# Performance work log

Measured on AMD Instinct MI355X. Metric: run time of the kernel, lower is better.

The kernel has to match this reference:

```python
import jax, jax.numpy as jnp
import numpy as np

NUM_LAYERS = 4
CODEBOOK_SIZE = 2048
DIM = 256
N = 32768
BETA = 0.25
EPS = 1e-12  # F.normalize eps


def setup_inputs() -> dict:
    key = jax.random.key(0)
    kx, kc = jax.random.split(key)
    x = jax.random.normal(kx, (N, DIM), dtype=jnp.float32)
    # nn.Embedding default init: N(0, 1)
    codebooks = jax.random.normal(kc, (NUM_LAYERS, CODEBOOK_SIZE, DIM), dtype=jnp.float32)
    return {"x": x, "codebooks": codebooks}


def reference(x, codebooks):
    sg = jax.lax.stop_gradient
    residual = x
    all_indices = []
    decoded = jnp.zeros_like(x)
    total_loss = jnp.zeros((), dtype=x.dtype)
    n_elem = x.size
    for layer in range(NUM_LAYERS):
        cb = codebooks[layer]                      # [K, D] (raw, used for gather)
        norm = jnp.linalg.norm(cb, axis=-1, keepdims=True)
        cbn = cb / jnp.maximum(norm, EPS)          # L2-normalized, used for distances
        # squared L2 distances; argmin is invariant to the sqrt in torch.cdist
        d2 = (
            jnp.sum(residual * residual, axis=-1, keepdims=True)
            - 2.0 * residual @ cbn.T
            + jnp.sum(cbn * cbn, axis=-1)
        )                                          # [N, K]
        idx = jnp.argmin(d2, axis=-1)              # [N]
        all_indices.append(idx)
        q = cb[idx]                                # [N, D] gather from RAW codebook
        codebook_loss = jnp.sum((residual - sg(q)) ** 2) / n_elem
        commitment_loss = jnp.sum((sg(residual) - q) ** 2) / n_elem
        total_loss = total_loss + codebook_loss + BETA * commitment_loss
        decoded = decoded + q
        # residual = residual - (residual + sg(q - residual)) == sg(residual - q)
        residual = sg(residual - q)
    stru_ids = jnp.stack(all_indices, axis=1)      # [N, L]
    return stru_ids, decoded, total_loss
```

## Files before the change

### kernel.cpp

```cpp
#include <hip/hip_runtime.h>
#include <math.h>

#define L_NUM 4
#define K_CB  2048
#define D_DIM 256
#define N_ROWS 32768
#define CAP 56
#define WACC  0.12f
#define WACC2 0.125f

typedef _Float16 half8 __attribute__((ext_vector_type(8)));
typedef _Float16 half4v __attribute__((ext_vector_type(4)));
typedef float f32x16 __attribute__((ext_vector_type(16)));

__device__ __forceinline__ void gl_lds16(const void* g, void* l) {
  __builtin_amdgcn_global_load_lds(
      (const __attribute__((address_space(1))) void*)g,
      (__attribute__((address_space(3))) void*)l, 16, 0, 0);
}
__device__ __forceinline__ unsigned fenc(float f) {
  unsigned u = __float_as_uint(f);
  return (u & 0x80000000u) ? ~u : (u | 0x80000000u);
}
__device__ __forceinline__ float fdec(unsigned k) {
  unsigned u = (k & 0x80000000u) ? (k ^ 0x80000000u) : ~k;
  return __uint_as_float(u);
}

__global__ __launch_bounds__(64)
void prep_all_kernel(const float* __restrict__ cb,
                     float* __restrict__ cbn,
                     _Float16* __restrict__ cb16) {
  const int b = blockIdx.x;
  const int k = b & 2047, l = b >> 11;
  const int lane = threadIdx.x;
  float4 v = reinterpret_cast<const float4*>(cb + (size_t)b * D_DIM)[lane];
  float s = v.x*v.x + v.y*v.y + v.z*v.z + v.w*v.w;
  #pragma unroll
  for (int m = 1; m < 64; m <<= 1) s += __shfl_xor(s, m, 64);
  const float den = fmaxf(sqrtf(s), 1e-12f);
  v.x /= den; v.y /= den; v.z /= den; v.w /= den;
  reinterpret_cast<float4*>(cbn + (size_t)b * D_DIM)[lane] = v;
  half4v h;
  h[0] = (_Float16)v.x; h[1] = (_Float16)v.y; h[2] = (_Float16)v.z; h[3] = (_Float16)v.w;
  const int tile = k >> 9, col = k & 511;
  const int kchunk = lane >> 3;
  const int sslot  = (lane >> 1) & 3;
  const int rem    = (lane & 1) * 4;
  const size_t off = (size_t)l * (K_CB * D_DIM)
                   + (size_t)(tile * 8 + kchunk) * 16384
                   + (size_t)sslot * 4096 + (size_t)col * 8 + rem;
  *(half4v*)(cb16 + off) = h;
}

__global__ __launch_bounds__(512, 2)
void rq_fused_kernel(const float* __restrict__ x,
                     const float* __restrict__ cb,
                     const float* __restrict__ cbn,
                     const _Float16* __restrict__ cb16,
                     float* __restrict__ out_ids,
                     float* __restrict__ out_dec,
                     double* __restrict__ dloss) {
  extern __shared__ char sm[];
  _Float16* A16   = (_Float16*)sm;
  _Float16* Bs    = (_Float16*)(sm + 65536);
  unsigned* cp    = (unsigned*)(sm + 131072);
  int*      cn    = (int*)(sm + 131072 + 128*CAP*4);
  unsigned* gmax  = (unsigned*)((char*)cn + 512);
  unsigned* bestp = (unsigned*)((char*)gmax + 512);

  const int t = threadIdx.x;
  const int wid = t >> 6, ln = t & 63;
  const int l31 = ln & 31, hl = ln >> 5;
  const int rowg = wid >> 2, colg = wid & 3;
  const int urow = t >> 2, qo = (t & 3) * 64;
  const int row0 = blockIdx.x * 128;
  const int mrow0 = rowg * 64 + l31, mrow1 = mrow0 + 32;

  float r[64];
  {
    const float4* xg = (const float4*)(x + (size_t)(row0 + urow) * D_DIM + qo);
    #pragma unroll
    for (int i = 0; i < 16; ++i) {
      const float4 a = xg[i];
      r[i*4+0]=a.x; r[i*4+1]=a.y; r[i*4+2]=a.z; r[i*4+3]=a.w;
    }
  }
  #pragma unroll
  for (int j = 0; j < 8; ++j) {
    half8 h;
    #pragma unroll
    for (int e = 0; e < 8; ++e) h[e] = (_Float16)r[j*8+e];
    const int slot = (t & 3) * 8 + j;
    *(half8*)(A16 + slot*1024 + urow*8) = h;
  }
  if (t < 128) { cn[t] = 0; gmax[t] = 0u; bestp[t] = 0u; }
  int id0 = 0, id1 = 0, id2 = 0, id3 = 0;
  double lloss = 0.0;

  #pragma unroll 1
  for (int l = 0; l < L_NUM; ++l) {
    const char* Bimg = (const char*)cb16 + (size_t)l * (K_CB * D_DIM * 2);
    {
      char* dst = (char*)Bs;
      #pragma unroll
      for (int i = 0; i < 4; ++i)
        gl_lds16(Bimg + t*16 + i*8192, dst + t*16 + i*8192);
    }
    __syncthreads();

    f32x16 acc[4][2];

    #pragma unroll 1
    for (int g = 0; g < 32; ++g) {
      if ((g & 7) == 0) {
        #pragma unroll
        for (int bi = 0; bi < 4; ++bi)
          #pragma unroll
          for (int ai = 0; ai < 2; ++ai)
            #pragma unroll
            for (int e = 0; e < 16; ++e) acc[bi][ai][e] = 0.f;
      }
      if (g < 31) {
        char* dst = (char*)Bs + ((g + 1) & 1) * 32768;
        const char* src = Bimg + (size_t)(g + 1) * 32768;
        #pragma unroll
        for (int i = 0; i < 4; ++i)
          gl_lds16(src + t*16 + i*8192, dst + t*16 + i*8192);
      }
      const _Float16* Bb = Bs + (g & 1) * 16384;
      const int cK = g & 7;
      #pragma unroll
      for (int ks2 = 0; ks2 < 2; ++ks2) {
        const int sa = cK*4 + ks2*2 + hl;
        const int sb = ks2*2 + hl;
        half8 af[2], bf[4];
        af[0] = *(const half8*)(A16 + sa*1024 + mrow0*8);
        af[1] = *(const half8*)(A16 + sa*1024 + mrow1*8);
        #pragma unroll
        for (int bi = 0; bi < 4; ++bi) {
          const int col = colg*128 + bi*32 + l31;
          bf[bi] = *(const half8*)(Bb + sb*4096 + col*8);
        }
        #pragma unroll
        for (int bi = 0; bi < 4; ++bi) {
          acc[bi][0] = __builtin_amdgcn_mfma_f32_32x32x16_f16(bf[bi], af[0], acc[bi][0], 0, 0, 0);
          acc[bi][1] = __builtin_amdgcn_mfma_f32_32x32x16_f16(bf[bi], af[1], acc[bi][1], 0, 0, 0);
        }
      }
      if ((g & 7) == 7) {
        const int ct = g >> 3;
        #pragma unroll
        for (int ai = 0; ai < 2; ++ai) {
          const int mrow = ai ? mrow1 : mrow0;
          float m = -INFINITY;
          #pragma unroll
          for (int bi = 0; bi < 4; ++bi)
            #pragma unroll
            for (int rg = 0; rg < 16; ++rg) m = fmaxf(m, acc[bi][ai][rg]);
          atomicMax(&gmax[mrow], fenc(m));
          const float thr = fdec(gmax[mrow]) - WACC;
          #pragma unroll
          for (int bi = 0; bi < 4; ++bi)
            #pragma unroll
            for (int rg = 0; rg < 16; ++rg) {
              const float v = acc[bi][ai][rg];
              if (v >= thr) {
                const unsigned q = (unsigned)((v + 64.f) * 16384.f);
                const unsigned cidx = (unsigned)(ct*512 + colg*128 + bi*32
                                                 + 4*hl + (rg & 3) + 8*(rg >> 2));
                const unsigned pk = (q << 11) | cidx;
                atomicMax(&bestp[mrow], pk);
                const int slot = atomicAdd(&cn[mrow], 1);
                if (slot < CAP) cp[mrow*CAP + slot] = pk;
              }
            }
        }
      }
      __syncthreads();
    }

    {
      const float thr2 = fdec(gmax[urow]) - WACC2;
      const int m = min(cn[urow], CAP);
      double bsc = (double)INFINITY; int bidx = 0x7fffffff;
      #pragma unroll 1
      for (int j = 0; j <= m; ++j) {
        const unsigned p = (j < m) ? cp[urow*CAP + j] : bestp[urow];
        const float v = (float)(p >> 11) * (1.f/16384.f) - 64.f;
        if (j < m && v < thr2) continue;
        const int cidx = (int)(p & 2047u);
        const float4* cpn = (const float4*)(cbn + ((size_t)l*K_CB + cidx)*D_DIM + qo);
        double s = 0.0, n2 = 0.0;
        #pragma unroll
        for (int i = 0; i < 16; ++i) {
          const float4 a = cpn[i];
          s  = fma((double)r[i*4+0], (double)a.x, s);
          s  = fma((double)r[i*4+1], (double)a.y, s);
          s  = fma((double)r[i*4+2], (double)a.z, s);
          s  = fma((double)r[i*4+3], (double)a.w, s);
          n2 = fma((double)a.x, (double)a.x, n2);
          n2 = fma((double)a.y, (double)a.y, n2);
          n2 = fma((double)a.z, (double)a.z, n2);
          n2 = fma((double)a.w, (double)a.w, n2);
        }
        s  += __shfl_xor(s, 1, 64);  s  += __shfl_xor(s, 2, 64);
        n2 += __shfl_xor(n2, 1, 64); n2 += __shfl_xor(n2, 2, 64);
        const double sc = -2.0 * s + n2;
        if (sc < bsc || (sc == bsc && cidx < bidx)) { bsc = sc; bidx = cidx; }
      }
      bidx &= 2047;
      if (l == 0) id0 = bidx; else if (l == 1) id1 = bidx;
      else if (l == 2) id2 = bidx; else id3 = bidx;
      if ((t & 3) == 0) out_ids[(size_t)(row0 + urow)*L_NUM + l] = (float)bidx;

      const float4* qg = (const float4*)(cb + ((size_t)l*K_CB + bidx)*D_DIM + qo);
      #pragma unroll
      for (int i = 0; i < 16; ++i) {
        const float4 q = qg[i];
        r[i*4+0] -= q.x; r[i*4+1] -= q.y; r[i*4+2] -= q.z; r[i*4+3] -= q.w;
        lloss += (double)r[i*4+0]*r[i*4+0] + (double)r[i*4+1]*r[i*4+1]
               + (double)r[i*4+2]*r[i*4+2] + (double)r[i*4+3]*r[i*4+3];
      }
      if (l < 3) {
        #pragma unroll
        for (int j = 0; j < 8; ++j) {
          half8 h;
          #pragma unroll
          for (int e = 0; e < 8; ++e) h[e] = (_Float16)r[j*8+e];
          const int slot = (t & 3) * 8 + j;
          *(half8*)(A16 + slot*1024 + urow*8) = h;
        }
      }
    }
    __syncthreads();
    if (l < 3 && t < 128) { cn[t] = 0; gmax[t] = 0u; bestp[t] = 0u; }
  }

  {
    float dec[64];
    #pragma unroll
    for (int l2 = 0; l2 < L_NUM; ++l2) {
      const int idl = (l2 == 0) ? id0 : (l2 == 1) ? id1 : (l2 == 2) ? id2 : id3;
      const float4* qg = (const float4*)(cb + ((size_t)l2*K_CB + idl)*D_DIM + qo);
      #pragma unroll
      for (int i = 0; i < 16; ++i) {
        const float4 q = qg[i];
        if (l2 == 0) { dec[i*4+0]=q.x; dec[i*4+1]=q.y; dec[i*4+2]=q.z; dec[i*4+3]=q.w; }
        else { dec[i*4+0]+=q.x; dec[i*4+1]+=q.y; dec[i*4+2]+=q.z; dec[i*4+3]+=q.w; }
      }
    }
    float4* dg = (float4*)(out_dec + (size_t)(row0 + urow)*D_DIM + qo);
    #pragma unroll
    for (int i = 0; i < 16; ++i)
      dg[i] = make_float4(dec[i*4+0], dec[i*4+1], dec[i*4+2], dec[i*4+3]);
  }

  double* lw = (double*)cp;
  #pragma unroll
  for (int m = 1; m < 64; m <<= 1) lloss += __shfl_xor(lloss, m, 64);
  if (ln == 0) lw[wid] = lloss;
  __syncthreads();
  if (t == 0) {
    double s2 = 0.0;
    #pragma unroll
    for (int j = 0; j < 8; ++j) s2 += lw[j];
    atomicAdd(dloss, s2);
  }
}

__global__ void rq_fin_kernel(const double* __restrict__ dls, float* __restrict__ out_loss) {
  out_loss[0] = (float)(dls[0] * 1.25 / 8388608.0);
}

extern "C" void kernel_launch(void* const* d_in, const int* in_sizes, int n_in,
                              void* d_out, int out_size, void* d_ws, size_t ws_size,
                              hipStream_t stream) {
  const float* x  = (const float*)d_in[0];
  const float* cb = (const float*)d_in[1];
  float* out      = (float*)d_out;
  float* out_ids  = out;
  float* out_dec  = out + (size_t)N_ROWS * L_NUM;
  float* out_loss = out_dec + (size_t)N_ROWS * D_DIM;

  char* w = (char*)d_ws;
  double* dls = (double*)w;                   w += 256;
  float* cbn = (float*)w;                     w += (size_t)L_NUM*K_CB*D_DIM*4;
  _Float16* cb16 = (_Float16*)w;              w += (size_t)L_NUM*K_CB*D_DIM*2;

  hipMemsetAsync(dls, 0, sizeof(double), stream);
  prep_all_kernel<<<L_NUM*K_CB, 64, 0, stream>>>(cb, cbn, cb16);

  const size_t smem = 65536 + 65536 + 128*CAP*4 + 512 + 512 + 512;
  hipFuncSetAttribute(reinterpret_cast<const void*>(rq_fused_kernel),
                      hipFuncAttributeMaxDynamicSharedMemorySize, (int)smem);
  rq_fused_kernel<<<N_ROWS/128, 512, smem, stream>>>(x, cb, cbn, cb16,
                                                     out_ids, out_dec, dls);
  rq_fin_kernel<<<1, 1, 0, stream>>>(dls, out_loss);
}
```

Before: 345.1 us.

## Halve block tile to 64 rows with 256 threads and 256-column B chunks

Reduces each block from 128 rows and 512 threads to 64 rows and 256 threads, with each wave computing a 32x128 tile (4 MFMA accumulators instead of 8). The codebook fp16 layout is reorganized into 256-column chunks of 16 KB, so the double-buffered B stage is halved and the loop runs 64 steps. Shared memory per block roughly halves and register pressure drops, which should allow more blocks per CU and better latency hiding. The cost is that every block still streams the full codebook per layer, so total L2/global traffic for B doubles and B reuse across rows halves, with more barriers per layer.

```diff
diff --git a/kernel.cpp b/kernel.cpp
--- a/kernel.cpp
+++ b/kernel.cpp
@@ -5,6 +5,7 @@
 #define K_CB  2048
 #define D_DIM 256
 #define N_ROWS 32768
+#define ROWS_B 64
 #define CAP 56
 #define WACC  0.12f
 #define WACC2 0.125f
@@ -43,17 +44,17 @@
   reinterpret_cast<float4*>(cbn + (size_t)b * D_DIM)[lane] = v;
   half4v h;
   h[0] = (_Float16)v.x; h[1] = (_Float16)v.y; h[2] = (_Float16)v.z; h[3] = (_Float16)v.w;
-  const int tile = k >> 9, col = k & 511;
-  const int kchunk = lane >> 3;
-  const int sslot  = (lane >> 1) & 3;
-  const int rem    = (lane & 1) * 4;
+  const int ct = k >> 8, col = k & 255;
+  const int kc    = lane >> 3;
+  const int sslot = (lane >> 1) & 3;
+  const int rem   = (lane & 1) * 4;
   const size_t off = (size_t)l * (K_CB * D_DIM)
-                   + (size_t)(tile * 8 + kchunk) * 16384
-                   + (size_t)sslot * 4096 + (size_t)col * 8 + rem;
+                   + (size_t)(ct * 8 + kc) * 8192
+                   + (size_t)sslot * 2048 + (size_t)col * 8 + rem;
   *(half4v*)(cb16 + off) = h;
 }
 
-__global__ __launch_bounds__(512, 2)
+__global__ __launch_bounds__(256, 2)
 void rq_fused_kernel(const float* __restrict__ x,
                      const float* __restrict__ cb,
                      const float* __restrict__ cbn,
@@ -63,19 +64,19 @@
                      double* __restrict__ dloss) {
   extern __shared__ char sm[];
   _Float16* A16   = (_Float16*)sm;
-  _Float16* Bs    = (_Float16*)(sm + 65536);
-  unsigned* cp    = (unsigned*)(sm + 131072);
-  int*      cn    = (int*)(sm + 131072 + 128*CAP*4);
-  unsigned* gmax  = (unsigned*)((char*)cn + 512);
-  unsigned* bestp = (unsigned*)((char*)gmax + 512);
+  _Float16* Bs    = (_Float16*)(sm + 32768);
+  unsigned* cp    = (unsigned*)(sm + 65536);
+  int*      cn    = (int*)(sm + 65536 + 64*CAP*4);
+  unsigned* gmax  = (unsigned*)((char*)cn + 256);
+  unsigned* bestp = (unsigned*)((char*)gmax + 256);
 
   const int t = threadIdx.x;
   const int wid = t >> 6, ln = t & 63;
   const int l31 = ln & 31, hl = ln >> 5;
-  const int rowg = wid >> 2, colg = wid & 3;
+  const int rowg = wid >> 1, colg = wid & 1;
   const int urow = t >> 2, qo = (t & 3) * 64;
-  const int row0 = blockIdx.x * 128;
-  const int mrow0 = rowg * 64 + l31, mrow1 = mrow0 + 32;
+  const int row0 = blockIdx.x * ROWS_B;
+  const int mrow = rowg * 32 + l31;
 
   float r[64];
   {
@@ -92,9 +93,9 @@
     #pragma unroll
     for (int e = 0; e < 8; ++e) h[e] = (_Float16)r[j*8+e];
     const int slot = (t & 3) * 8 + j;
-    *(half8*)(A16 + slot*1024 + urow*8) = h;
-  }
-  if (t < 128) { cn[t] = 0; gmax[t] = 0u; bestp[t] = 0u; }
+    *(half8*)(A16 + slot*512 + urow*8) = h;
+  }
+  if (t < 64) { cn[t] = 0; gmax[t] = 0u; bestp[t] = 0u; }
   int id0 = 0, id1 = 0, id2 = 0, id3 = 0;
   double lloss = 0.0;
 
@@ -105,77 +106,71 @@
       char* dst = (char*)Bs;
       #pragma unroll
       for (int i = 0; i < 4; ++i)
-        gl_lds16(Bimg + t*16 + i*8192, dst + t*16 + i*8192);
+        gl_lds16(Bimg + t*16 + i*4096, dst + t*16 + i*4096);
     }
     __syncthreads();
 
-    f32x16 acc[4][2];
+    f32x16 acc[4];
 
     #pragma unroll 1
-    for (int g = 0; g < 32; ++g) {
+    for (int g = 0; g < 64; ++g) {
       if ((g & 7) == 0) {
         #pragma unroll
         for (int bi = 0; bi < 4; ++bi)
           #pragma unroll
-          for (int ai = 0; ai < 2; ++ai)
-            #pragma unroll
-            for (int e = 0; e < 16; ++e) acc[bi][ai][e] = 0.f;
-      }
-      if (g < 31) {
-        char* dst = (char*)Bs + ((g + 1) & 1) * 32768;
-        const char* src = Bimg + (size_t)(g + 1) * 32768;
+          for (int e = 0; e < 16; ++e) acc[bi][e] = 0.f;
+      }
+      if (g < 63) {
+        char* dst = (char*)Bs + ((g + 1) & 1) * 16384;
+        const char* src = Bimg + (size_t)(g + 1) * 16384;
         #pragma unroll
         for (int i = 0; i < 4; ++i)
-          gl_lds16(src + t*16 + i*8192, dst + t*16 + i*8192);
-      }
-      const _Float16* Bb = Bs + (g & 1) * 16384;
-      const int cK = g & 7;
+          gl_lds16(src + t*16 + i*4096, dst + t*16 + i*4096);
+      }
+      const _Float16* Bb = Bs + (g & 1) * 8192;
+      const int kc = g & 7;
       #pragma unroll
       for (int ks2 = 0; ks2 < 2; ++ks2) {
-        const int sa = cK*4 + ks2*2 + hl;
         const int sb = ks2*2 + hl;
-        half8 af[2], bf[4];
-        af[0] = *(const half8*)(A16 + sa*1024 + mrow0*8);
-        af[1] = *(const half8*)(A16 + sa*1024 + mrow1*8);
-        #pragma unroll
-        for (int bi = 0; bi < 4; ++bi) {
-          const int col = colg*128 + bi*32 + l31;
-          bf[bi] = *(const half8*)(Bb + sb*4096 + col*8);
-        }
-        #pragma unroll
-        for (int bi = 0; bi < 4; ++bi) {
-          acc[bi][0] = __builtin_amdgcn_mfma_f32_32x32x16_f16(bf[bi], af[0], acc[bi][0], 0, 0, 0);
-          acc[bi][1] = __builtin_amdgcn_mfma_f32_32x32x16_f16(bf[bi], af[1], acc[bi][1], 0, 0, 0);
-        }
+        const int sa = kc*4 + sb;
+        const half8 af = *(const half8*)(A16 + sa*512 + mrow*8);
+        half8 bf[4];
+        #pragma unroll
+        for (int bi = 0; bi < 4; ++bi)
+          bf[bi] = *(const half8*)(Bb + sb*2048 + (colg*128 + bi*32 + l31)*8);
+        #pragma unroll
+        for (int bi = 0; bi < 4; ++bi)
+          acc[bi] = __builtin_amdgcn_mfma_f32_32x32x16_f16(bf[bi], af, acc[bi], 0, 0, 0);
       }
       if ((g & 7) == 7) {
         const int ct = g >> 3;
-        #pragma unroll
-        for (int ai = 0; ai < 2; ++ai) {
-          const int mrow = ai ? mrow1 : mrow0;
-          float m = -INFINITY;
+        float m4[4];
+        #pragma unroll
+        for (int bi = 0; bi < 4; ++bi) {
+          float m0 = fmaxf(fmaxf(acc[bi][0], acc[bi][1]), fmaxf(acc[bi][2], acc[bi][3]));
+          float m1 = fmaxf(fmaxf(acc[bi][4], acc[bi][5]), fmaxf(acc[bi][6], acc[bi][7]));
+          float m2 = fmaxf(fmaxf(acc[bi][8], acc[bi][9]), fmaxf(acc[bi][10], acc[bi][11]));
+          float m3 = fmaxf(fmaxf(acc[bi][12], acc[bi][13]), fmaxf(acc[bi][14], acc[bi][15]));
+          m4[bi] = fmaxf(fmaxf(m0, m1), fmaxf(m2, m3));
+        }
+        const float m = fmaxf(fmaxf(m4[0], m4[1]), fmaxf(m4[2], m4[3]));
+        atomicMax(&gmax[mrow], fenc(m));
+        const float thr = fdec(gmax[mrow]) - WACC;
+        #pragma unroll
+        for (int bi = 0; bi < 4; ++bi)
           #pragma unroll
-          for (int bi = 0; bi < 4; ++bi)
-            #pragma unroll
-            for (int rg = 0; rg < 16; ++rg) m = fmaxf(m, acc[bi][ai][rg]);
-          atomicMax(&gmax[mrow], fenc(m));
-          const float thr = fdec(gmax[mrow]) - WACC;
-          #pragma unroll
-          for (int bi = 0; bi < 4; ++bi)
-            #pragma unroll
-            for (int rg = 0; rg < 16; ++rg) {
-              const float v = acc[bi][ai][rg];
-              if (v >= thr) {
-                const unsigned q = (unsigned)((v + 64.f) * 16384.f);
-                const unsigned cidx = (unsigned)(ct*512 + colg*128 + bi*32
-                                                 + 4*hl + (rg & 3) + 8*(rg >> 2));
-                const unsigned pk = (q << 11) | cidx;
-                atomicMax(&bestp[mrow], pk);
-                const int slot = atomicAdd(&cn[mrow], 1);
-                if (slot < CAP) cp[mrow*CAP + slot] = pk;
-              }
+          for (int rg = 0; rg < 16; ++rg) {
+            const float v = acc[bi][rg];
+            if (v >= thr) {
+              const unsigned q = (unsigned)((v + 64.f) * 16384.f);
+              const unsigned cidx = (unsigned)(ct*256 + colg*128 + bi*32
+                                               + 4*hl + (rg & 3) + 8*(rg >> 2));
+              const unsigned pk = (q << 11) | cidx;
+              atomicMax(&bestp[mrow], pk);
+              const int slot = atomicAdd(&cn[mrow], 1);
+              if (slot < CAP) cp[mrow*CAP + slot] = pk;
             }
-        }
+          }
       }
       __syncthreads();
     }
@@ -229,12 +224,12 @@
           #pragma unroll
           for (int e = 0; e < 8; ++e) h[e] = (_Float16)r[j*8+e];
           const int slot = (t & 3) * 8 + j;
-          *(half8*)(A16 + slot*1024 + urow*8) = h;
+          *(half8*)(A16 + slot*512 + urow*8) = h;
         }
       }
     }
     __syncthreads();
-    if (l < 3 && t < 128) { cn[t] = 0; gmax[t] = 0u; bestp[t] = 0u; }
+    if (l < 3 && t < 64) { cn[t] = 0; gmax[t] = 0u; bestp[t] = 0u; }
   }
 
   {
@@ -261,12 +256,7 @@
   for (int m = 1; m < 64; m <<= 1) lloss += __shfl_xor(lloss, m, 64);
   if (ln == 0) lw[wid] = lloss;
   __syncthreads();
-  if (t == 0) {
-    double s2 = 0.0;
-    #pragma unroll
-    for (int j = 0; j < 8; ++j) s2 += lw[j];
-    atomicAdd(dloss, s2);
-  }
+  if (t == 0) atomicAdd(dloss, lw[0] + lw[1] + lw[2] + lw[3]);
 }
 
 __global__ void rq_fin_kernel(const double* __restrict__ dls, float* __restrict__ out_loss) {
@@ -291,10 +281,10 @@
   hipMemsetAsync(dls, 0, sizeof(double), stream);
   prep_all_kernel<<<L_NUM*K_CB, 64, 0, stream>>>(cb, cbn, cb16);
 
-  const size_t smem = 65536 + 65536 + 128*CAP*4 + 512 + 512 + 512;
+  const size_t smem = 32768 + 32768 + 64*CAP*4 + 256 + 256 + 256;
   hipFuncSetAttribute(reinterpret_cast<const void*>(rq_fused_kernel),
                       hipFuncAttributeMaxDynamicSharedMemorySize, (int)smem);
-  rq_fused_kernel<<<N_ROWS/128, 512, smem, stream>>>(x, cb, cbn, cb16,
-                                                     out_ids, out_dec, dls);
+  rq_fused_kernel<<<N_ROWS/ROWS_B, 256, smem, stream>>>(x, cb, cbn, cb16,
+                                                        out_ids, out_dec, dls);
   rq_fin_kernel<<<1, 1, 0, stream>>>(dls, out_loss);
 }
```

Measured after the change: 352.8 us. 2.2% more time.

## Drop persistent residual registers, recompute residual, use split barriers with vmcnt waits

Applied to the files above, without the earlier changes.

Stops keeping the 64-float residual in registers across the whole GEMM loop and instead reloads x and subtracts the previously chosen raw codebook rows before the refinement step, cutting register pressure during the MFMA loop. The per-tile __syncthreads is replaced with raw s_barrier pairs and explicit s_waitcnt vmcnt so the next tile's global-to-LDS prefetch stays in flight. Candidate capacity is lowered from 56 to 40 to shrink LDS. The cost is extra global reads of x and codebook rows per layer, plus a higher chance that the candidate list overflows.

```diff
diff --git a/kernel.cpp b/kernel.cpp
--- a/kernel.cpp
+++ b/kernel.cpp
@@ -5,7 +5,8 @@
 #define K_CB  2048
 #define D_DIM 256
 #define N_ROWS 32768
-#define CAP 56
+#define ROWS_B 128
+#define CAP 40
 #define WACC  0.12f
 #define WACC2 0.125f
 
@@ -43,14 +44,38 @@
   reinterpret_cast<float4*>(cbn + (size_t)b * D_DIM)[lane] = v;
   half4v h;
   h[0] = (_Float16)v.x; h[1] = (_Float16)v.y; h[2] = (_Float16)v.z; h[3] = (_Float16)v.w;
-  const int tile = k >> 9, col = k & 511;
-  const int kchunk = lane >> 3;
-  const int sslot  = (lane >> 1) & 3;
-  const int rem    = (lane & 1) * 4;
+  const int ct = k >> 9, col = k & 511;
+  const int kc    = lane >> 3;
+  const int sslot = (lane >> 1) & 3;
+  const int rem   = (lane & 1) * 4;
   const size_t off = (size_t)l * (K_CB * D_DIM)
-                   + (size_t)(tile * 8 + kchunk) * 16384
+                   + (size_t)(ct * 8 + kc) * 16384
                    + (size_t)sslot * 4096 + (size_t)col * 8 + rem;
   *(half4v*)(cb16 + off) = h;
+}
+
+#define COLL(ACC, BI, MROW, THR, CT) \
+  _Pragma("unroll") \
+  for (int rg = 0; rg < 16; ++rg) { \
+    const float v_ = (ACC)[rg]; \
+    if (v_ >= (THR)) { \
+      const unsigned q_ = (unsigned)((v_ + 64.f) * 16384.f); \
+      const unsigned ci_ = (unsigned)((CT)*512 + colg*128 + (BI)*32 \
+                                      + 4*hl + (rg & 3) + 8*(rg >> 2)); \
+      const unsigned pk_ = (q_ << 11) | ci_; \
+      atomicMax(&bestp[(MROW)], pk_); \
+      const int slot_ = atomicAdd(&cn[(MROW)], 1); \
+      if (slot_ < CAP) cp[(MROW)*CAP + slot_] = pk_; \
+    } \
+  }
+
+__device__ __forceinline__ float vmax16_4(const f32x16& a, const f32x16& b,
+                                          const f32x16& c, const f32x16& d) {
+  float m = -INFINITY;
+  #pragma unroll
+  for (int i = 0; i < 16; ++i)
+    m = fmaxf(m, fmaxf(fmaxf(a[i], b[i]), fmaxf(c[i], d[i])));
+  return m;
 }
 
 __global__ __launch_bounds__(512, 2)
@@ -74,25 +99,20 @@
   const int l31 = ln & 31, hl = ln >> 5;
   const int rowg = wid >> 2, colg = wid & 3;
   const int urow = t >> 2, qo = (t & 3) * 64;
-  const int row0 = blockIdx.x * 128;
-  const int mrow0 = rowg * 64 + l31, mrow1 = mrow0 + 32;
-
-  float r[64];
+  const int row0 = blockIdx.x * ROWS_B;
+  const int mrowA = rowg * 64 + l31;
+
   {
     const float4* xg = (const float4*)(x + (size_t)(row0 + urow) * D_DIM + qo);
     #pragma unroll
-    for (int i = 0; i < 16; ++i) {
-      const float4 a = xg[i];
-      r[i*4+0]=a.x; r[i*4+1]=a.y; r[i*4+2]=a.z; r[i*4+3]=a.w;
-    }
-  }
-  #pragma unroll
-  for (int j = 0; j < 8; ++j) {
-    half8 h;
-    #pragma unroll
-    for (int e = 0; e < 8; ++e) h[e] = (_Float16)r[j*8+e];
-    const int slot = (t & 3) * 8 + j;
-    *(half8*)(A16 + slot*1024 + urow*8) = h;
+    for (int j = 0; j < 8; ++j) {
+      const float4 a = xg[j*2], b = xg[j*2+1];
+      half8 h;
+      h[0]=(_Float16)a.x; h[1]=(_Float16)a.y; h[2]=(_Float16)a.z; h[3]=(_Float16)a.w;
+      h[4]=(_Float16)b.x; h[5]=(_Float16)b.y; h[6]=(_Float16)b.z; h[7]=(_Float16)b.w;
+      const int slot = (t & 3) * 8 + j;
+      *(half8*)(A16 + slot*1024 + urow*8) = h;
+    }
   }
   if (t < 128) { cn[t] = 0; gmax[t] = 0u; bestp[t] = 0u; }
   int id0 = 0, id1 = 0, id2 = 0, id3 = 0;
@@ -101,86 +121,100 @@
   #pragma unroll 1
   for (int l = 0; l < L_NUM; ++l) {
     const char* Bimg = (const char*)cb16 + (size_t)l * (K_CB * D_DIM * 2);
+    __syncthreads();
     {
-      char* dst = (char*)Bs;
       #pragma unroll
       for (int i = 0; i < 4; ++i)
-        gl_lds16(Bimg + t*16 + i*8192, dst + t*16 + i*8192);
-    }
-    __syncthreads();
-
-    f32x16 acc[4][2];
+        gl_lds16(Bimg + t*16 + i*8192, (char*)Bs + t*16 + i*8192);
+    }
+
+    f32x16 a00, a01, a10, a11, a20, a21, a30, a31;
 
     #pragma unroll 1
     for (int g = 0; g < 32; ++g) {
-      if ((g & 7) == 0) {
-        #pragma unroll
-        for (int bi = 0; bi < 4; ++bi)
-          #pragma unroll
-          for (int ai = 0; ai < 2; ++ai)
-            #pragma unroll
-            for (int e = 0; e < 16; ++e) acc[bi][ai][e] = 0.f;
-      }
+      __builtin_amdgcn_s_barrier();
       if (g < 31) {
         char* dst = (char*)Bs + ((g + 1) & 1) * 32768;
         const char* src = Bimg + (size_t)(g + 1) * 32768;
         #pragma unroll
         for (int i = 0; i < 4; ++i)
           gl_lds16(src + t*16 + i*8192, dst + t*16 + i*8192);
+        asm volatile("s_waitcnt vmcnt(4)" ::: "memory");
+      } else {
+        asm volatile("s_waitcnt vmcnt(0)" ::: "memory");
+      }
+      __builtin_amdgcn_s_barrier();
+
+      if ((g & 7) == 0) {
+        #pragma unroll
+        for (int e = 0; e < 16; ++e) {
+          a00[e]=0.f; a01[e]=0.f; a10[e]=0.f; a11[e]=0.f;
+          a20[e]=0.f; a21[e]=0.f; a30[e]=0.f; a31[e]=0.f;
+        }
       }
       const _Float16* Bb = Bs + (g & 1) * 16384;
-      const int cK = g & 7;
+      const int kc = g & 7;
       #pragma unroll
       for (int ks2 = 0; ks2 < 2; ++ks2) {
-        const int sa = cK*4 + ks2*2 + hl;
         const int sb = ks2*2 + hl;
-        half8 af[2], bf[4];
-        af[0] = *(const half8*)(A16 + sa*1024 + mrow0*8);
-        af[1] = *(const half8*)(A16 + sa*1024 + mrow1*8);
-        #pragma unroll
-        for (int bi = 0; bi < 4; ++bi) {
-          const int col = colg*128 + bi*32 + l31;
-          bf[bi] = *(const half8*)(Bb + sb*4096 + col*8);
-        }
-        #pragma unroll
-        for (int bi = 0; bi < 4; ++bi) {
-          acc[bi][0] = __builtin_amdgcn_mfma_f32_32x32x16_f16(bf[bi], af[0], acc[bi][0], 0, 0, 0);
-          acc[bi][1] = __builtin_amdgcn_mfma_f32_32x32x16_f16(bf[bi], af[1], acc[bi][1], 0, 0, 0);
-        }
+        const int sa = kc*4 + sb;
+        const half8 af0 = *(const half8*)(A16 + sa*1024 + mrowA*8);
+        const half8 af1 = *(const half8*)(A16 + sa*1024 + (mrowA + 32)*8);
+        const half8 bf0 = *(const half8*)(Bb + sb*4096 + (colg*128 +  0 + l31)*8);
+        const half8 bf1 = *(const half8*)(Bb + sb*4096 + (colg*128 + 32 + l31)*8);
+        const half8 bf2 = *(const half8*)(Bb + sb*4096 + (colg*128 + 64 + l31)*8);
+        const half8 bf3 = *(const half8*)(Bb + sb*4096 + (colg*128 + 96 + l31)*8);
+        a00 = __builtin_amdgcn_mfma_f32_32x32x16_f16(bf0, af0, a00, 0, 0, 0);
+        a01 = __builtin_amdgcn_mfma_f32_32x32x16_f16(bf0, af1, a01, 0, 0, 0);
+        a10 = __builtin_amdgcn_mfma_f32_32x32x16_f16(bf1, af0, a10, 0, 0, 0);
+        a11 = __builtin_amdgcn_mfma_f32_32x32x16_f16(bf1, af1, a11, 0, 0, 0);
+        a20 = __builtin_amdgcn_mfma_f32_32x32x16_f16(bf2, af0, a20, 0, 0, 0);
+        a21 = __builtin_amdgcn_mfma_f32_32x32x16_f16(bf2, af1, a21, 0, 0, 0);
+        a30 = __builtin_amdgcn_mfma_f32_32x32x16_f16(bf3, af0, a30, 0, 0, 0);
+        a31 = __builtin_amdgcn_mfma_f32_32x32x16_f16(bf3, af1, a31, 0, 0, 0);
       }
       if ((g & 7) == 7) {
         const int ct = g >> 3;
-        #pragma unroll
-        for (int ai = 0; ai < 2; ++ai) {
-          const int mrow = ai ? mrow1 : mrow0;
-          float m = -INFINITY;
-          #pragma unroll
-          for (int bi = 0; bi < 4; ++bi)
-            #pragma unroll
-            for (int rg = 0; rg < 16; ++rg) m = fmaxf(m, acc[bi][ai][rg]);
-          atomicMax(&gmax[mrow], fenc(m));
+        {
+          const int mrow = mrowA;
+          const float mm = vmax16_4(a00, a10, a20, a30);
+          atomicMax(&gmax[mrow], fenc(mm));
           const float thr = fdec(gmax[mrow]) - WACC;
-          #pragma unroll
-          for (int bi = 0; bi < 4; ++bi)
-            #pragma unroll
-            for (int rg = 0; rg < 16; ++rg) {
-              const float v = acc[bi][ai][rg];
-              if (v >= thr) {
-                const unsigned q = (unsigned)((v + 64.f) * 16384.f);
-                const unsigned cidx = (unsigned)(ct*512 + colg*128 + bi*32
-                                                 + 4*hl + (rg & 3) + 8*(rg >> 2));
-                const unsigned pk = (q << 11) | cidx;
-                atomicMax(&bestp[mrow], pk);
-                const int slot = atomicAdd(&cn[mrow], 1);
-                if (slot < CAP) cp[mrow*CAP + slot] = pk;
-              }
-            }
-        }
-      }
-      __syncthreads();
-    }
+          COLL(a00, 0, mrow, thr, ct) COLL(a10, 1, mrow, thr, ct)
+          COLL(a20, 2, mrow, thr, ct) COLL(a30, 3, mrow, thr, ct)
+        }
+        {
+          const int mrow = mrowA + 32;
+          const float mm = vmax16_4(a01, a11, a21, a31);
+          atomicMax(&gmax[mrow], fenc(mm));
+          const float thr = fdec(gmax[mrow]) - WACC;
+          COLL(a01, 0, mrow, thr, ct) COLL(a11, 1, mrow, thr, ct)
+          COLL(a21, 2, mrow, thr, ct) COLL(a31, 3, mrow, thr, ct)
+        }
+      }
+    }
+    __syncthreads();
 
     {
+      float r[64];
+      {
+        const float4* xg = (const float4*)(x + (size_t)(row0 + urow)*D_DIM + qo);
+        #pragma unroll
+        for (int i = 0; i < 16; ++i) {
+          const float4 a = xg[i];
+          r[i*4+0]=a.x; r[i*4+1]=a.y; r[i*4+2]=a.z; r[i*4+3]=a.w;
+        }
+      }
+      #pragma unroll 1
+      for (int j = 0; j < l; ++j) {
+        const int pj = (j==0) ? id0 : (j==1) ? id1 : (j==2) ? id2 : id3;
+        const float4* qg = (const float4*)(cb + ((size_t)j*K_CB + pj)*D_DIM + qo);
+        #pragma unroll
+        for (int i = 0; i < 16; ++i) {
+          const float4 a = qg[i];
+          r[i*4+0]-=a.x; r[i*4+1]-=a.y; r[i*4+2]-=a.z; r[i*4+3]-=a.w;
+        }
+      }
       const float thr2 = fdec(gmax[urow]) - WACC2;
       const int m = min(cn[urow], CAP);
       double bsc = (double)INFINITY; int bidx = 0x7fffffff;
@@ -294,7 +328,7 @@
   const size_t smem = 65536 + 65536 + 128*CAP*4 + 512 + 512 + 512;
   hipFuncSetAttribute(reinterpret_cast<const void*>(rq_fused_kernel),
                       hipFuncAttributeMaxDynamicSharedMemorySize, (int)smem);
-  rq_fused_kernel<<<N_ROWS/128, 512, smem, stream>>>(x, cb, cbn, cb16,
-                                                     out_ids, out_dec, dls);
+  rq_fused_kernel<<<N_ROWS/ROWS_B, 512, smem, stream>>>(x, cb, cbn, cb16,
+                                                        out_ids, out_dec, dls);
   rq_fin_kernel<<<1, 1, 0, stream>>>(dls, out_loss);
 }
```

Result: slower. 389.8 us (+12.9%).
